# Kernel tuning notes

Measured on AMD Instinct MI355X. Metric: run time of the kernel, lower is better.

## Reference

```python
import jax, jax.numpy as jnp
import numpy as np

# Matcher hyperparameters (from __init__ defaults)
COST_CLASS = 1.0
COST_CENTER = 5.0
COST_IOU = 2.0
CENTER_THRESHOLD = 2.0
INF_REPLACE = 1000000.0

B, Q, N, NUM_CLASSES = 64, 4096, 256, 20
SCENE_EXTENT = 50.0  # meters; box centers uniform in [0, 50]


def setup_inputs() -> dict:
    key = jax.random.key(0)
    k1, k2, k3, k4, k5, k6 = jax.random.split(key, 6)
    pred_logits = jax.random.normal(k1, (B, Q, NUM_CLASSES + 1), dtype=jnp.float32)
    pred_centers = jax.random.uniform(k2, (B, Q, 3), dtype=jnp.float32) * SCENE_EXTENT
    pred_sizes = jax.random.uniform(k3, (B, Q, 3), dtype=jnp.float32) * 2.5 + 0.5
    pred_boxes = jnp.concatenate([pred_centers, pred_sizes], axis=-1)  # [B,Q,6]
    tgt_centers = jax.random.uniform(k4, (B, N, 3), dtype=jnp.float32) * SCENE_EXTENT
    tgt_sizes = jax.random.uniform(k5, (B, N, 3), dtype=jnp.float32) * 2.5 + 0.5
    target_boxes = jnp.concatenate([tgt_centers, tgt_sizes], axis=-1)  # [B,N,6]
    target_labels = jax.random.randint(k6, (B, N), 0, NUM_CLASSES)  # all valid fg classes
    return {
        "pred_logits": pred_logits,
        "pred_boxes": pred_boxes,
        "target_labels": target_labels,
        "target_boxes": target_boxes,
    }


def _pairwise_iou3d(pred_boxes, target_boxes):
    # pred_boxes [B,Q,6], target_boxes [B,N,6] -> iou [B,Q,N]
    c1, s1 = pred_boxes[..., :3], pred_boxes[..., 3:]
    c2, s2 = target_boxes[..., :3], target_boxes[..., 3:]
    min1 = (c1 - s1 * 0.5)[:, :, None, :]  # [B,Q,1,3]
    max1 = (c1 + s1 * 0.5)[:, :, None, :]
    min2 = (c2 - s2 * 0.5)[:, None, :, :]  # [B,1,N,3]
    max2 = (c2 + s2 * 0.5)[:, None, :, :]
    inter_size = jnp.clip(jnp.minimum(max1, max2) - jnp.maximum(min1, min2), 0.0)
    inter_vol = jnp.prod(inter_size, axis=-1)  # [B,Q,N]
    vol1 = jnp.prod(s1, axis=-1)[:, :, None]  # [B,Q,1]
    vol2 = jnp.prod(s2, axis=-1)[:, None, :]  # [B,1,N]
    union = vol1 + vol2 - inter_vol
    return jnp.where(union > 0, inter_vol / union, 0.0)


def reference(pred_logits, pred_boxes, target_labels, target_boxes):
    # Class cost: -softmax prob of the target's class (foreground classes only)
    probs_fg = jax.nn.softmax(pred_logits, axis=-1)[..., :-1]  # [B,Q,C]
    class_cost = -jax.vmap(lambda p, l: p[:, l])(probs_fg, target_labels)  # [B,Q,N]

    # Center distance cost with threshold gating (torch.cdist = euclidean)
    pc = pred_boxes[..., :3]
    tc = target_boxes[..., :3]
    dist = jnp.sqrt(jnp.sum((pc[:, :, None, :] - tc[:, None, :, :]) ** 2, axis=-1))
    center_cost = jnp.where(dist <= CENTER_THRESHOLD, dist, jnp.inf)

    # 3D IoU cost
    iou_cost = 1.0 - _pairwise_iou3d(pred_boxes, target_boxes)

    total = COST_CLASS * class_cost + COST_CENTER * center_cost + COST_IOU * iou_cost
    total = jnp.where(jnp.isinf(total), INF_REPLACE, total)
    return total  # [B,Q,N] cost matrix fed to the (CPU) Hungarian solver
```

## Files before the change

kernel.cpp:

```cpp
#include <hip/hip_runtime.h>
#include <math.h>

#define BQ 64
#define QQ 4096
#define NN 256
#define NC 20
#define NL 21
#define TQ 256
#define GEO_STRIDE 12
#define PROB_STRIDE 257

#define GATE_D2  0x1.000001p+2f
#define CULL_D2  4.03f

__global__ __launch_bounds__(256)
void matcher_kernel(const float* __restrict__ logits,
                    const float* __restrict__ pboxes,
                    const int*   __restrict__ tlabels,
                    const float* __restrict__ tboxes,
                    float* __restrict__ out) {
    __shared__ __align__(16) float geo[TQ * GEO_STRIDE];
    __shared__ float prob[NC * PROB_STRIDE];
    const int tid = threadIdx.x;
    const int b   = blockIdx.y;
    const int q0  = blockIdx.x * TQ;

    {
        const int q = q0 + tid;
        const float* lg = logits + (size_t)(b * QQ + q) * NL;
        float l[NL];
        #pragma unroll
        for (int c = 0; c < NL; ++c) l[c] = lg[c];
        float m = l[0];
        #pragma unroll
        for (int c = 1; c < NL; ++c) m = fmaxf(m, l[c]);
        float e[NL];
        float s = 0.f;
        #pragma unroll
        for (int c = 0; c < NL; ++c) { e[c] = expf(l[c] - m); s += e[c]; }
        const float rs = 1.0f / s;
        #pragma unroll
        for (int c = 0; c < NC; ++c)
            prob[c * PROB_STRIDE + tid] = -(e[c] * rs);

        const float* pb = pboxes + (size_t)(b * QQ + q) * 6;
        const float pcx = pb[0], pcy = pb[1], pcz = pb[2];
        const float psx = pb[3], psy = pb[4], psz = pb[5];
        float4* gp = (float4*)(geo + tid * GEO_STRIDE);
        gp[0] = make_float4(pcx, pcy, pcz, pcx * pcx + pcy * pcy + pcz * pcz);
        gp[1] = make_float4(pcx - psx * 0.5f, pcy - psy * 0.5f, pcz - psz * 0.5f,
                            psx * psy * psz);
        gp[2] = make_float4(pcx + psx * 0.5f, pcy + psy * 0.5f, pcz + psz * 0.5f, 0.f);
    }

    const int lane = tid & 63;
    const int w    = tid >> 6;
    const int n0   = lane * 4;
    float tcx[4], tcy[4], tcz[4];
    float n2x[4], n2y[4], n2z[4], t2[4];
    float mn_x[4], mn_y[4], mn_z[4], mx_x[4], mx_y[4], mx_z[4], v2[4];
    int plab[4];
    #pragma unroll
    for (int j = 0; j < 4; ++j) {
        const float* tb = tboxes + (size_t)(b * NN + n0 + j) * 6;
        const float cx = tb[0], cy = tb[1], cz = tb[2];
        const float sx = tb[3], sy = tb[4], sz = tb[5];
        tcx[j] = cx; tcy[j] = cy; tcz[j] = cz;
        n2x[j] = -2.0f * cx; n2y[j] = -2.0f * cy; n2z[j] = -2.0f * cz;
        t2[j]  = cx * cx + cy * cy + cz * cz;
        mn_x[j] = cx - sx * 0.5f; mn_y[j] = cy - sy * 0.5f; mn_z[j] = cz - sz * 0.5f;
        mx_x[j] = cx + sx * 0.5f; mx_y[j] = cy + sy * 0.5f; mx_z[j] = cz + sz * 0.5f;
        v2[j]   = sx * sy * sz;
        plab[j] = tlabels[b * NN + n0 + j] * PROB_STRIDE;
    }

    __syncthreads();

    const float4 MISS = make_float4(1000000.0f, 1000000.0f, 1000000.0f, 1000000.0f);
    float* ob = out + ((size_t)(b * QQ + q0)) * NN + n0;

    for (int qq = w; qq < TQ; qq += 4) {
        const float4* gp = (const float4*)(geo + qq * GEO_STRIDE);
        const float4 g0 = gp[0];

        int near = 0;
        #pragma unroll
        for (int j = 0; j < 4; ++j) {
            const float d2f = fmaf(g0.x, n2x[j],
                             fmaf(g0.y, n2y[j],
                             fmaf(g0.z, n2z[j], g0.w + t2[j])));
            near |= (d2f <= CULL_D2);
        }

        float4* orow = (float4*)(ob + (size_t)qq * NN);
        if (!__any(near)) {
            *orow = MISS;
            continue;
        }

        const float4 g1 = gp[1];
        const float4 g2 = gp[2];
        float r[4];
        #pragma unroll
        for (int j = 0; j < 4; ++j) {
            const float dx = __fsub_rn(g0.x, tcx[j]);
            const float dy = __fsub_rn(g0.y, tcy[j]);
            const float dz = __fsub_rn(g0.z, tcz[j]);
            const float d2 = __fadd_rn(__fadd_rn(__fmul_rn(dx, dx), __fmul_rn(dy, dy)),
                                       __fmul_rn(dz, dz));
            const float negp = prob[plab[j] + qq];
            const float dist = __builtin_amdgcn_sqrtf(d2);

            const float ix = fmaxf(fminf(g2.x, mx_x[j]) - fmaxf(g1.x, mn_x[j]), 0.f);
            const float iy = fmaxf(fminf(g2.y, mx_y[j]) - fmaxf(g1.y, mn_y[j]), 0.f);
            const float iz = fmaxf(fminf(g2.z, mx_z[j]) - fmaxf(g1.z, mn_z[j]), 0.f);
            const float iv  = ix * iy * iz;
            const float uni = g1.w + v2[j] - iv;
            const float iou = iv * __builtin_amdgcn_rcpf(uni);

            const float t = fmaf(5.0f, dist, negp) + fmaf(-2.0f, iou, 2.0f);
            r[j] = (d2 <= GATE_D2) ? t : 1000000.0f;
        }
        *orow = make_float4(r[0], r[1], r[2], r[3]);
    }
}

extern "C" void kernel_launch(void* const* d_in, const int* in_sizes, int n_in,
                              void* d_out, int out_size, void* d_ws, size_t ws_size,
                              hipStream_t stream) {
    const float* logits  = (const float*)d_in[0];
    const float* pboxes  = (const float*)d_in[1];
    const int*   tlabels = (const int*)d_in[2];
    const float* tboxes  = (const float*)d_in[3];
    float* out = (float*)d_out;

    dim3 grid(QQ / TQ, BQ);
    matcher_kernel<<<grid, dim3(256), 0, stream>>>(logits, pboxes, tlabels, tboxes, out);
}
```

Measured before the change: 295.5 us.

## Halve query tile, cut registers, prefetch geometry and use nontemporal stores

Result: slower. 304.5 us (+3.0%).

```diff
diff --git a/kernel.cpp b/kernel.cpp
--- a/kernel.cpp
+++ b/kernel.cpp
@@ -6,14 +6,16 @@
 #define NN 256
 #define NC 20
 #define NL 21
-#define TQ 256
+#define TQ 128
 #define GEO_STRIDE 12
-#define PROB_STRIDE 257
+#define PROB_STRIDE (TQ + 1)
 
 #define GATE_D2  0x1.000001p+2f
 #define CULL_D2  4.03f
 
-__global__ __launch_bounds__(256)
+typedef float v4f __attribute__((ext_vector_type(4)));
+
+__global__ __launch_bounds__(256, 6)
 void matcher_kernel(const float* __restrict__ logits,
                     const float* __restrict__ pboxes,
                     const int*   __restrict__ tlabels,
@@ -25,7 +27,7 @@
     const int b   = blockIdx.y;
     const int q0  = blockIdx.x * TQ;
 
-    {
+    if (tid < TQ) {
         const int q = q0 + tid;
         const float* lg = logits + (size_t)(b * QQ + q) * NL;
         float l[NL];
@@ -56,32 +58,28 @@
     const int lane = tid & 63;
     const int w    = tid >> 6;
     const int n0   = lane * 4;
-    float tcx[4], tcy[4], tcz[4];
     float n2x[4], n2y[4], n2z[4], t2[4];
-    float mn_x[4], mn_y[4], mn_z[4], mx_x[4], mx_y[4], mx_z[4], v2[4];
+    float szx[4], szy[4], szz[4];
     int plab[4];
     #pragma unroll
     for (int j = 0; j < 4; ++j) {
         const float* tb = tboxes + (size_t)(b * NN + n0 + j) * 6;
         const float cx = tb[0], cy = tb[1], cz = tb[2];
-        const float sx = tb[3], sy = tb[4], sz = tb[5];
-        tcx[j] = cx; tcy[j] = cy; tcz[j] = cz;
         n2x[j] = -2.0f * cx; n2y[j] = -2.0f * cy; n2z[j] = -2.0f * cz;
         t2[j]  = cx * cx + cy * cy + cz * cz;
-        mn_x[j] = cx - sx * 0.5f; mn_y[j] = cy - sy * 0.5f; mn_z[j] = cz - sz * 0.5f;
-        mx_x[j] = cx + sx * 0.5f; mx_y[j] = cy + sy * 0.5f; mx_z[j] = cz + sz * 0.5f;
-        v2[j]   = sx * sy * sz;
+        szx[j] = tb[3]; szy[j] = tb[4]; szz[j] = tb[5];
         plab[j] = tlabels[b * NN + n0 + j] * PROB_STRIDE;
     }
 
     __syncthreads();
 
-    const float4 MISS = make_float4(1000000.0f, 1000000.0f, 1000000.0f, 1000000.0f);
+    const v4f MISS = 1000000.0f;
     float* ob = out + ((size_t)(b * QQ + q0)) * NN + n0;
 
+    float4 g0 = *(const float4*)(geo + w * GEO_STRIDE);
     for (int qq = w; qq < TQ; qq += 4) {
-        const float4* gp = (const float4*)(geo + qq * GEO_STRIDE);
-        const float4 g0 = gp[0];
+        const int qn = (qq + 4) & (TQ - 1);
+        const float4 g0n = *(const float4*)(geo + qn * GEO_STRIDE);
 
         int near = 0;
         #pragma unroll
@@ -92,36 +90,46 @@
             near |= (d2f <= CULL_D2);
         }
 
-        float4* orow = (float4*)(ob + (size_t)qq * NN);
+        v4f* orow = (v4f*)(ob + (size_t)qq * NN);
         if (!__any(near)) {
-            *orow = MISS;
+            __builtin_nontemporal_store(MISS, orow);
+            g0 = g0n;
             continue;
         }
 
-        const float4 g1 = gp[1];
-        const float4 g2 = gp[2];
-        float r[4];
+        const float4 g1 = *(const float4*)(geo + qq * GEO_STRIDE + 4);
+        const float4 g2 = *(const float4*)(geo + qq * GEO_STRIDE + 8);
+        v4f r;
         #pragma unroll
         for (int j = 0; j < 4; ++j) {
-            const float dx = __fsub_rn(g0.x, tcx[j]);
-            const float dy = __fsub_rn(g0.y, tcy[j]);
-            const float dz = __fsub_rn(g0.z, tcz[j]);
+            const float tcx = -0.5f * n2x[j];
+            const float tcy = -0.5f * n2y[j];
+            const float tcz = -0.5f * n2z[j];
+            const float dx = __fsub_rn(g0.x, tcx);
+            const float dy = __fsub_rn(g0.y, tcy);
+            const float dz = __fsub_rn(g0.z, tcz);
             const float d2 = __fadd_rn(__fadd_rn(__fmul_rn(dx, dx), __fmul_rn(dy, dy)),
                                        __fmul_rn(dz, dz));
             const float negp = prob[plab[j] + qq];
             const float dist = __builtin_amdgcn_sqrtf(d2);
 
-            const float ix = fmaxf(fminf(g2.x, mx_x[j]) - fmaxf(g1.x, mn_x[j]), 0.f);
-            const float iy = fmaxf(fminf(g2.y, mx_y[j]) - fmaxf(g1.y, mn_y[j]), 0.f);
-            const float iz = fmaxf(fminf(g2.z, mx_z[j]) - fmaxf(g1.z, mn_z[j]), 0.f);
+            const float mnx = tcx - szx[j] * 0.5f, mxx = tcx + szx[j] * 0.5f;
+            const float mny = tcy - szy[j] * 0.5f, mxy = tcy + szy[j] * 0.5f;
+            const float mnz = tcz - szz[j] * 0.5f, mxz = tcz + szz[j] * 0.5f;
+            const float ix = fmaxf(fminf(g2.x, mxx) - fmaxf(g1.x, mnx), 0.f);
+            const float iy = fmaxf(fminf(g2.y, mxy) - fmaxf(g1.y, mny), 0.f);
+            const float iz = fmaxf(fminf(g2.z, mxz) - fmaxf(g1.z, mnz), 0.f);
             const float iv  = ix * iy * iz;
-            const float uni = g1.w + v2[j] - iv;
+            const float uni = g1.w + szx[j] * szy[j] * szz[j] - iv;
             const float iou = iv * __builtin_amdgcn_rcpf(uni);
 
             const float t = fmaf(5.0f, dist, negp) + fmaf(-2.0f, iou, 2.0f);
-            r[j] = (d2 <= GATE_D2) ? t : 1000000.0f;
+            const float rv = (d2 <= GATE_D2) ? t : 1000000.0f;
+            if (j == 0) r.x = rv; else if (j == 1) r.y = rv;
+            else if (j == 2) r.z = rv; else r.w = rv;
         }
-        *orow = make_float4(r[0], r[1], r[2], r[3]);
+        __builtin_nontemporal_store(r, orow);
+        g0 = g0n;
     }
 }
 
```
